# Kernel tuning notes

Measured on AMD Instinct MI355X. Metric: run time of the kernel, lower is better.

The kernel has to match this reference:

```python
import jax, jax.numpy as jnp
import numpy as np

B, L, D, M = 32, 512, 768, 24  # batch, max_len, bert hidden, mentions per sample
MAX_SPAN = 16


def setup_inputs() -> dict:
    key = jax.random.key(0)
    k1, k2, k3, k4 = jax.random.split(key, 4)
    sequence_output = jax.random.normal(k1, (B, L, D), dtype=jnp.float32)
    head_indexes = jax.random.randint(k2, (B, L), 0, L)
    starts = jax.random.randint(k3, (B, M), 0, L - MAX_SPAN)
    lens = jax.random.randint(k4, (B, M), 1, MAX_SPAN)
    entity_mentions = jnp.stack([starts, starts + lens], axis=-1)  # [B, M, 2], start < end
    return {
        "sequence_output": sequence_output,
        "head_indexes": head_indexes,
        "entity_mentions": entity_mentions,
    }


def reference(sequence_output, head_indexes, entity_mentions):
    b, l, d = sequence_output.shape
    m = entity_mentions.shape[1]

    # per-sample head-token gather: seq[i] = seq[i][head_indexes[i]]
    seq = jnp.take_along_axis(sequence_output, head_indexes[..., None], axis=1)  # [B, L, D]

    # span mean-pool via exclusive prefix sums: mean(seq[s:e]) = (cs[e]-cs[s])/(e-s)
    cs = jnp.concatenate(
        [jnp.zeros((b, 1, d), seq.dtype), jnp.cumsum(seq, axis=1)], axis=1
    )  # [B, L+1, D]
    starts = entity_mentions[..., 0]  # [B, M]
    ends = entity_mentions[..., 1]    # [B, M]
    span_sum = (
        jnp.take_along_axis(cs, ends[..., None], axis=1)
        - jnp.take_along_axis(cs, starts[..., None], axis=1)
    )  # [B, M, D]
    pooled = span_sum / (ends - starts)[..., None].astype(seq.dtype)  # [B, M, D]

    # all ordered pairs i != j (eval path order: i outer, j inner, skip i==j)
    ii, jj = np.meshgrid(np.arange(m), np.arange(m), indexing="ij")
    offdiag = ii != jj
    ii = jnp.asarray(ii[offdiag])  # [P]
    jj = jnp.asarray(jj[offdiag])  # [P]
    p = ii.shape[0]

    obj = pooled[:, ii]  # [B, P, D]
    sub = pooled[:, jj]  # [B, P, D]
    relation_predictions = jnp.concatenate([obj, sub], axis=-1).reshape(b * p, 2 * d)

    batch_idx = jnp.repeat(jnp.arange(b), p)  # [B*P]
    pairs = jnp.stack(
        [
            batch_idx,
            starts[:, ii].reshape(-1),
            ends[:, ii].reshape(-1),
            starts[:, jj].reshape(-1),
            ends[:, jj].reshape(-1),
        ],
        axis=-1,
    )  # [B*P, 5] = [idx, obj_start, obj_end, subj_start, subj_end]
    return relation_predictions, pairs
```

## Files before the change

kernel.cpp:

```cpp
#include <hip/hip_runtime.h>

#define B 32
#define L 512
#define D 768
#define M 24
#define P (M * (M - 1))
#define Q4 (D / 4)
#define MPB 3
#define NBLK (B * M / MPB)

typedef float f32x4 __attribute__((ext_vector_type(4)));

__global__ void __launch_bounds__(2 * Q4)
fused_kernel(const float* __restrict__ seq,
             const int*   __restrict__ head,
             const int*   __restrict__ em,
             float*       __restrict__ out)
{
    int bk = blockIdx.x;
    int t  = threadIdx.x;
    int hf = t >= Q4;
    int tq = hf ? t - Q4 : t;

    int bm0 = bk * MPB;
    int b   = bm0 / M;
    int m0  = bm0 - b * M;

    const float* seqb  = seq  + (size_t)b * L * D;
    const int*   headb = head + b * L;
    const int*   emb   = em   + b * M * 2;

    f32x4* outq = (f32x4*)out;
    float* pout = out + (size_t)B * P * 2 * D;
    size_t rowbase = (size_t)b * P;

    int s = emb[2 * m0], e = emb[2 * m0 + 1];
    int len = e - s;
    f32x4 acc = (f32x4)(0.f);
    {
        int hidx[15];
        #pragma unroll
        for (int r = 0; r < 15; ++r) {
            int l = s + r; l = (l < e) ? l : s;
            hidx[r] = headb[l];
        }
        f32x4 vv[15];
        #pragma unroll
        for (int r = 0; r < 15; ++r)
            vv[r] = ((const f32x4*)(seqb + (size_t)hidx[r] * D))[tq];
        #pragma unroll
        for (int r = 0; r < 15; ++r)
            acc += (r < len) ? vv[r] : (f32x4)(0.f);
    }

    #pragma unroll
    for (int k = 0; k < MPB; ++k) {
        int m = m0 + k;
        f32x4 v = acc * (1.0f / (float)len);

        int s_n = 0, e_n = 0, len_n = 0;
        int hidx[15];
        f32x4 vv[15];
        if (k + 1 < MPB) {
            s_n = emb[2 * (m + 1)]; e_n = emb[2 * (m + 1) + 1];
            len_n = e_n - s_n;
            #pragma unroll
            for (int r = 0; r < 15; ++r) {
                int l = s_n + r; l = (l < e_n) ? l : s_n;
                hidx[r] = headb[l];
            }
            #pragma unroll
            for (int r = 0; r < 15; ++r)
                vv[r] = ((const f32x4*)(seqb + (size_t)hidx[r] * D))[tq];
        }

        if (!hf) {
            size_t q = (rowbase + (size_t)m * 23) * 384 + tq;
            #pragma unroll
            for (int r = 0; r < 23; ++r) {
                __builtin_nontemporal_store(v, &outq[q]);
                q += 384;
            }
            if (tq < 23) {
                int r = tq;
                int j = (r < m) ? r : r + 1;
                float* o = pout + (rowbase + (size_t)m * 23 + r) * 5;
                o[0] = (float)b;
                o[1] = (float)s;
                o[2] = (float)e;
                o[3] = (float)emb[2 * j];
                o[4] = (float)emb[2 * j + 1];
            }
        } else {
            #pragma unroll
            for (int i = 0; i < M; ++i) {
                if (i == m) continue;
                int r = (m < i) ? m : m - 1;
                size_t row = rowbase + (size_t)i * 23 + r;
                __builtin_nontemporal_store(v, &outq[row * 384 + Q4 + tq]);
            }
        }

        if (k + 1 < MPB) {
            acc = (f32x4)(0.f);
            #pragma unroll
            for (int r = 0; r < 15; ++r)
                acc += (r < len_n) ? vv[r] : (f32x4)(0.f);
            s = s_n; e = e_n; len = len_n;
        }
    }
}

extern "C" void kernel_launch(void* const* d_in, const int* in_sizes, int n_in,
                              void* d_out, int out_size, void* d_ws, size_t ws_size,
                              hipStream_t stream) {
    const float* seq  = (const float*)d_in[0];
    const int*   head = (const int*)d_in[1];
    const int*   em   = (const int*)d_in[2];
    float* out = (float*)d_out;

    fused_kernel<<<NBLK, 2 * Q4, 0, stream>>>(seq, head, em, out);
}
```

Before: 28.76 us.

## Split obj/sub halves into separate blocks, two mentions per block

```diff
diff --git a/kernel.cpp b/kernel.cpp
--- a/kernel.cpp
+++ b/kernel.cpp
@@ -6,107 +6,112 @@
 #define M 24
 #define P (M * (M - 1))
 #define Q4 (D / 4)
-#define MPB 3
-#define NBLK (B * M / MPB)
 
 typedef float f32x4 __attribute__((ext_vector_type(4)));
 
-__global__ void __launch_bounds__(2 * Q4)
+__global__ void __launch_bounds__(Q4)
 fused_kernel(const float* __restrict__ seq,
              const int*   __restrict__ head,
              const int*   __restrict__ em,
              float*       __restrict__ out)
 {
-    int bk = blockIdx.x;
-    int t  = threadIdx.x;
-    int hf = t >= Q4;
-    int tq = hf ? t - Q4 : t;
-
-    int bm0 = bk * MPB;
-    int b   = bm0 / M;
-    int m0  = bm0 - b * M;
+    int blk  = blockIdx.x;
+    int half = blk & 1;
+    int g    = blk >> 1;
+    int b    = g / (M / 2);
+    int mp   = g - b * (M / 2);
+    int m0   = 2 * mp, m1 = m0 + 1;
+    int tq   = threadIdx.x;
 
     const float* seqb  = seq  + (size_t)b * L * D;
     const int*   headb = head + b * L;
     const int*   emb   = em   + b * M * 2;
 
+    int s0 = emb[2 * m0], e0 = emb[2 * m0 + 1];
+    int s1 = emb[2 * m1], e1 = emb[2 * m1 + 1];
+    int len0 = e0 - s0, len1 = e1 - s1;
+
+    int h0[15], h1[15];
+    #pragma unroll
+    for (int r = 0; r < 15; ++r) {
+        int l = s0 + r; l = (l < e0) ? l : s0;
+        h0[r] = headb[l];
+    }
+    #pragma unroll
+    for (int r = 0; r < 15; ++r) {
+        int l = s1 + r; l = (l < e1) ? l : s1;
+        h1[r] = headb[l];
+    }
+
+    f32x4 vv[15];
+    #pragma unroll
+    for (int r = 0; r < 15; ++r)
+        vv[r] = ((const f32x4*)(seqb + (size_t)h0[r] * D))[tq];
+    f32x4 acc = (f32x4)(0.f);
+    #pragma unroll
+    for (int r = 0; r < 15; ++r)
+        acc += (r < len0) ? vv[r] : (f32x4)(0.f);
+    f32x4 v0 = acc * (1.0f / (float)len0);
+
+    #pragma unroll
+    for (int r = 0; r < 15; ++r)
+        vv[r] = ((const f32x4*)(seqb + (size_t)h1[r] * D))[tq];
+
     f32x4* outq = (f32x4*)out;
     float* pout = out + (size_t)B * P * 2 * D;
     size_t rowbase = (size_t)b * P;
 
-    int s = emb[2 * m0], e = emb[2 * m0 + 1];
-    int len = e - s;
-    f32x4 acc = (f32x4)(0.f);
-    {
-        int hidx[15];
+    if (half == 0) {
+        size_t q = (rowbase + (size_t)m0 * 23) * 384 + tq;
         #pragma unroll
-        for (int r = 0; r < 15; ++r) {
-            int l = s + r; l = (l < e) ? l : s;
-            hidx[r] = headb[l];
+        for (int r = 0; r < 23; ++r) {
+            __builtin_nontemporal_store(v0, &outq[q]);
+            q += 384;
         }
-        f32x4 vv[15];
+        if (tq < 23) {
+            int r = tq;
+            int j = (r < m0) ? r : r + 1;
+            float* o = pout + (rowbase + (size_t)m0 * 23 + r) * 5;
+            o[0] = (float)b; o[1] = (float)s0; o[2] = (float)e0;
+            o[3] = (float)emb[2 * j]; o[4] = (float)emb[2 * j + 1];
+        }
+    } else {
         #pragma unroll
-        for (int r = 0; r < 15; ++r)
-            vv[r] = ((const f32x4*)(seqb + (size_t)hidx[r] * D))[tq];
-        #pragma unroll
-        for (int r = 0; r < 15; ++r)
-            acc += (r < len) ? vv[r] : (f32x4)(0.f);
+        for (int i = 0; i < M; ++i) {
+            if (i == m0) continue;
+            int r = (m0 < i) ? m0 : m0 - 1;
+            size_t row = rowbase + (size_t)i * 23 + r;
+            __builtin_nontemporal_store(v0, &outq[row * 384 + Q4 + tq]);
+        }
     }
 
+    acc = (f32x4)(0.f);
     #pragma unroll
-    for (int k = 0; k < MPB; ++k) {
-        int m = m0 + k;
-        f32x4 v = acc * (1.0f / (float)len);
+    for (int r = 0; r < 15; ++r)
+        acc += (r < len1) ? vv[r] : (f32x4)(0.f);
+    f32x4 v1 = acc * (1.0f / (float)len1);
 
-        int s_n = 0, e_n = 0, len_n = 0;
-        int hidx[15];
-        f32x4 vv[15];
-        if (k + 1 < MPB) {
-            s_n = emb[2 * (m + 1)]; e_n = emb[2 * (m + 1) + 1];
-            len_n = e_n - s_n;
-            #pragma unroll
-            for (int r = 0; r < 15; ++r) {
-                int l = s_n + r; l = (l < e_n) ? l : s_n;
-                hidx[r] = headb[l];
-            }
-            #pragma unroll
-            for (int r = 0; r < 15; ++r)
-                vv[r] = ((const f32x4*)(seqb + (size_t)hidx[r] * D))[tq];
+    if (half == 0) {
+        size_t q = (rowbase + (size_t)m1 * 23) * 384 + tq;
+        #pragma unroll
+        for (int r = 0; r < 23; ++r) {
+            __builtin_nontemporal_store(v1, &outq[q]);
+            q += 384;
         }
-
-        if (!hf) {
-            size_t q = (rowbase + (size_t)m * 23) * 384 + tq;
-            #pragma unroll
-            for (int r = 0; r < 23; ++r) {
-                __builtin_nontemporal_store(v, &outq[q]);
-                q += 384;
-            }
-            if (tq < 23) {
-                int r = tq;
-                int j = (r < m) ? r : r + 1;
-                float* o = pout + (rowbase + (size_t)m * 23 + r) * 5;
-                o[0] = (float)b;
-                o[1] = (float)s;
-                o[2] = (float)e;
-                o[3] = (float)emb[2 * j];
-                o[4] = (float)emb[2 * j + 1];
-            }
-        } else {
-            #pragma unroll
-            for (int i = 0; i < M; ++i) {
-                if (i == m) continue;
-                int r = (m < i) ? m : m - 1;
-                size_t row = rowbase + (size_t)i * 23 + r;
-                __builtin_nontemporal_store(v, &outq[row * 384 + Q4 + tq]);
-            }
+        if (tq < 23) {
+            int r = tq;
+            int j = (r < m1) ? r : r + 1;
+            float* o = pout + (rowbase + (size_t)m1 * 23 + r) * 5;
+            o[0] = (float)b; o[1] = (float)s1; o[2] = (float)e1;
+            o[3] = (float)emb[2 * j]; o[4] = (float)emb[2 * j + 1];
         }
-
-        if (k + 1 < MPB) {
-            acc = (f32x4)(0.f);
-            #pragma unroll
-            for (int r = 0; r < 15; ++r)
-                acc += (r < len_n) ? vv[r] : (f32x4)(0.f);
-            s = s_n; e = e_n; len = len_n;
+    } else {
+        #pragma unroll
+        for (int i = 0; i < M; ++i) {
+            if (i == m1) continue;
+            int r = (m1 < i) ? m1 : m1 - 1;
+            size_t row = rowbase + (size_t)i * 23 + r;
+            __builtin_nontemporal_store(v1, &outq[row * 384 + Q4 + tq]);
         }
     }
 }
@@ -119,5 +124,5 @@
     const int*   em   = (const int*)d_in[2];
     float* out = (float*)d_out;
 
-    fused_kernel<<<NBLK, 2 * Q4, 0, stream>>>(seq, head, em, out);
+    fused_kernel<<<B * M, Q4, 0, stream>>>(seq, head, em, out);
 }
```

Result: slower. 29.36 us (+2.1%).
